# Kernel optimization log

Measured on AMD Instinct MI355X. Metric: run time of the kernel, lower is better.

Reference implementation:

```python
import jax, jax.numpy as jnp
import numpy as np
import math

E, H, FFN, NQ = 1024, 16, 4096, 8
B, T = 2, 2048
EPS = 1e-5

def layernorm(x, g, b):
    mu = jnp.mean(x, axis=-1, keepdims=True)
    var = jnp.mean(jnp.square(x - mu), axis=-1, keepdims=True)
    return (x - mu) * jax.lax.rsqrt(var + EPS) * g + b

def setup_inputs() -> dict:
    key = jax.random.key(0)
    ks = jax.random.split(key, 8)
    x = jax.random.normal(ks[0], (B, T, E), dtype=jnp.float32)
    mask = jnp.ones((B, T, T), dtype=bool)
    # constant quantum measurement output: PauliZ expectations of a fixed
    # RandomLayer circuit applied to |0..0> (independent of the input tokens)
    q_out = jax.random.uniform(ks[1], (NQ,), minval=-1.0, maxval=1.0, dtype=jnp.float32)
    s1 = 1.0 / math.sqrt(NQ)
    w1 = jax.random.uniform(ks[2], (NQ, FFN), minval=-s1, maxval=s1, dtype=jnp.float32)
    b1 = jnp.zeros((FFN,), dtype=jnp.float32)
    s2 = 1.0 / math.sqrt(FFN)
    w2 = jax.random.uniform(ks[3], (FFN, E), minval=-s2, maxval=s2, dtype=jnp.float32)
    b2 = jnp.zeros((E,), dtype=jnp.float32)
    g1 = jnp.ones((E,), dtype=jnp.float32); be1 = jnp.zeros((E,), dtype=jnp.float32)
    g2 = jnp.ones((E,), dtype=jnp.float32); be2 = jnp.zeros((E,), dtype=jnp.float32)
    return dict(x=x, mask=mask, q_out=q_out, w1=w1, b1=b1, w2=w2, b2=b2,
                g1=g1, be1=be1, g2=g2, be2=be2)

def reference(x, mask, q_out, w1, b1, w2, b2, g1, be1, g2, be2):
    b, t, e = x.shape
    d_k = e // H
    # q = k = v = head-split x (module has no QKV projections)
    q = x.reshape(b, t, H, d_k).transpose(0, 2, 1, 3)  # [B,H,T,d_k]
    scores = jnp.einsum('bhqd,bhkd->bhqk', q, q) / math.sqrt(d_k)
    scores = jnp.where(mask[:, None, :, :], scores, -1e9)
    attn = jax.nn.softmax(scores, axis=-1)
    out = jnp.einsum('bhqk,bhkd->bhqd', attn, q)
    attn_out = out.transpose(0, 2, 1, 3).reshape(b, t, e)
    x1 = layernorm(x + attn_out, g1, be1)
    # quantum FFN: constant measurement vector broadcast over all tokens
    h = jnp.broadcast_to(q_out, (b, t, NQ))
    h = jnp.dot(h, w1) + b1
    ffn_out = jnp.dot(jax.nn.relu(h), w2) + b2
    return layernorm(x1 + ffn_out, g2, be2)
```

## Files before the change

### kernel.cpp

```cpp
#include <hip/hip_runtime.h>

#define E_   1024
#define H_   16
#define DK_  64
#define FFN_ 4096
#define NQ_  8
#define B_   2
#define T_   2048
#define QBLK 64
#define KVBLK 64
#define NT_  (T_ / KVBLK)

#define NPART 256
#define ROWS_PER_PART (FFN_ / NPART)

typedef __attribute__((ext_vector_type(8))) __bf16 bf16x8;
typedef __attribute__((ext_vector_type(4))) float f32x4;

__device__ __forceinline__ __bf16 tobf(float f) { return (__bf16)f; }

__device__ __forceinline__ unsigned pk2(float a, float b) {
  union { __bf16 h; unsigned short u; } ua, ub;
  ua.h = (__bf16)a; ub.h = (__bf16)b;
  return (unsigned)ua.u | ((unsigned)ub.u << 16);
}

__global__ __launch_bounds__(256)
void cvt_kernel(const float* __restrict__ x, __bf16* __restrict__ xbf) {
  const size_t base = ((size_t)blockIdx.x * 256 + threadIdx.x) * 8;
  float4 a = *reinterpret_cast<const float4*>(x + base);
  float4 b = *reinterpret_cast<const float4*>(x + base + 4);
  bf16x8 v;
  v[0] = tobf(a.x); v[1] = tobf(a.y); v[2] = tobf(a.z); v[3] = tobf(a.w);
  v[4] = tobf(b.x); v[5] = tobf(b.y); v[6] = tobf(b.z); v[7] = tobf(b.w);
  *reinterpret_cast<bf16x8*>(xbf + base) = v;
}

__global__ __launch_bounds__(256)
void ffn_part_kernel(const float* __restrict__ q_out, const float* __restrict__ w1,
                     const float* __restrict__ b1, const float* __restrict__ w2,
                     float* __restrict__ part) {
  __shared__ float h[ROWS_PER_PART];
  const int tid = threadIdx.x;
  const int p = blockIdx.x;
  const int f0 = p * ROWS_PER_PART;
  if (tid < ROWS_PER_PART) {
    const int f = f0 + tid;
    float a = b1[f];
#pragma unroll
    for (int n = 0; n < NQ_; ++n) a += q_out[n] * w1[n * FFN_ + f];
    h[tid] = fmaxf(a, 0.f);
  }
  __syncthreads();
  float4 acc = {0.f, 0.f, 0.f, 0.f};
#pragma unroll
  for (int j = 0; j < ROWS_PER_PART; ++j) {
    const float hf = h[j];
    float4 w = reinterpret_cast<const float4*>(w2 + (size_t)(f0 + j) * E_)[tid];
    acc.x += hf * w.x; acc.y += hf * w.y; acc.z += hf * w.z; acc.w += hf * w.w;
  }
  reinterpret_cast<float4*>(part + (size_t)p * E_)[tid] = acc;
}

__global__ __launch_bounds__(256)
void ffn_reduce_kernel(const float* __restrict__ part, const float* __restrict__ b2,
                       float* __restrict__ ffn_c) {
  const int e = blockIdx.x * 256 + threadIdx.x;
  float a = b2[e];
  for (int r = 0; r < NPART; ++r) a += part[(size_t)r * E_ + e];
  ffn_c[e] = a;
}

__global__ __launch_bounds__(128)
void attn_kernel(const __bf16* __restrict__ xbf, float* __restrict__ out) {
  __shared__ __bf16 Kt[KVBLK][DK_ + 8];
  __shared__ __bf16 VtF[DK_ * KVBLK];
  __shared__ __bf16 Pl[2][32][DK_ + 8];

  const int tid  = threadIdx.x;
  const int wave = tid >> 6;
  const int lane = tid & 63;
  const int l16  = lane & 15;
  const int lhi  = lane >> 4;

  const int bh = blockIdx.y;
  const int b  = bh >> 4;
  const int h  = bh & 15;
  const int qbase = blockIdx.x * QBLK;
  const __bf16* xb = xbf + (size_t)b * T_ * E_ + h * DK_;

  bf16x8 qa[2][2];
  {
    const __bf16 sc = (__bf16)0.125f;
#pragma unroll
    for (int g = 0; g < 2; ++g) {
      const __bf16* qrow = xb + (size_t)(qbase + wave * 32 + g * 16 + l16) * E_;
      bf16x8 v0 = *reinterpret_cast<const bf16x8*>(qrow + lhi * 8);
      bf16x8 v1 = *reinterpret_cast<const bf16x8*>(qrow + 32 + lhi * 8);
#pragma unroll
      for (int j = 0; j < 8; ++j) { v0[j] *= sc; v1[j] *= sc; }
      qa[g][0] = v0; qa[g][1] = v1;
    }
  }

  f32x4 acc[2][4];
#pragma unroll
  for (int g = 0; g < 2; ++g)
#pragma unroll
    for (int td = 0; td < 4; ++td) acc[g][td] = (f32x4){0.f, 0.f, 0.f, 0.f};
  float lg0 = 0.f, lg1 = 0.f;

  const int kp = tid >> 3;
  const int d0 = (tid & 7) * 8;
  const __bf16* kvbase = xb + (size_t)(4 * kp) * E_ + d0;

  uint4 pr[4];
#pragma unroll
  for (int r = 0; r < 4; ++r)
    pr[r] = *reinterpret_cast<const uint4*>(kvbase + (size_t)r * E_);

  for (int t = 0; t < NT_; ++t) {
    __syncthreads();
    {
#pragma unroll
      for (int r = 0; r < 4; ++r)
        *reinterpret_cast<uint4*>(&Kt[4 * kp + r][d0]) = pr[r];
      union U4 { uint4 v; unsigned short s[8]; } u0, u1, u2, u3;
      u0.v = pr[0]; u1.v = pr[1]; u2.v = pr[2]; u3.v = pr[3];
#pragma unroll
      for (int j = 0; j < 8; ++j) {
        const int d = d0 + j;
        uint2 w;
        w.x = (unsigned)u0.s[j] | ((unsigned)u1.s[j] << 16);
        w.y = (unsigned)u2.s[j] | ((unsigned)u3.s[j] << 16);
        const int byte = d * 128 + ((8 * kp) ^ ((((d & 7) ^ ((d >> 3) & 7))) << 4));
        *reinterpret_cast<uint2*>(reinterpret_cast<char*>(VtF) + byte) = w;
      }
    }
    if (t + 1 < NT_) {
      const __bf16* nb = kvbase + (size_t)(t + 1) * KVBLK * E_;
#pragma unroll
      for (int r = 0; r < 4; ++r)
        pr[r] = *reinterpret_cast<const uint4*>(nb + (size_t)r * E_);
    }
    __syncthreads();

    f32x4 s0[4], s1[4];
#pragma unroll
    for (int tn = 0; tn < 4; ++tn) {
      bf16x8 ka0 = *reinterpret_cast<const bf16x8*>(&Kt[tn * 16 + l16][lhi * 8]);
      bf16x8 ka1 = *reinterpret_cast<const bf16x8*>(&Kt[tn * 16 + l16][32 + lhi * 8]);
      f32x4 c0 = (f32x4){0.f, 0.f, 0.f, 0.f};
      c0 = __builtin_amdgcn_mfma_f32_16x16x32_bf16(ka0, qa[0][0], c0, 0, 0, 0);
      c0 = __builtin_amdgcn_mfma_f32_16x16x32_bf16(ka1, qa[0][1], c0, 0, 0, 0);
      s0[tn] = c0;
      f32x4 c1 = (f32x4){0.f, 0.f, 0.f, 0.f};
      c1 = __builtin_amdgcn_mfma_f32_16x16x32_bf16(ka0, qa[1][0], c1, 0, 0, 0);
      c1 = __builtin_amdgcn_mfma_f32_16x16x32_bf16(ka1, qa[1][1], c1, 0, 0, 0);
      s1[tn] = c1;
    }

#pragma unroll
    for (int tn = 0; tn < 4; ++tn) {
      float p0 = __expf(s0[tn][0]), p1 = __expf(s0[tn][1]);
      float p2 = __expf(s0[tn][2]), p3 = __expf(s0[tn][3]);
      lg0 += (p0 + p1) + (p2 + p3);
      uint2 w; w.x = pk2(p0, p1); w.y = pk2(p2, p3);
      *reinterpret_cast<uint2*>(&Pl[wave][l16][tn * 16 + lhi * 4]) = w;
    }
#pragma unroll
    for (int tn = 0; tn < 4; ++tn) {
      float p0 = __expf(s1[tn][0]), p1 = __expf(s1[tn][1]);
      float p2 = __expf(s1[tn][2]), p3 = __expf(s1[tn][3]);
      lg1 += (p0 + p1) + (p2 + p3);
      uint2 w; w.x = pk2(p0, p1); w.y = pk2(p2, p3);
      *reinterpret_cast<uint2*>(&Pl[wave][16 + l16][tn * 16 + lhi * 4]) = w;
    }
    asm volatile("s_waitcnt lgkmcnt(0)" ::: "memory");

#pragma unroll
    for (int kb = 0; kb < 2; ++kb) {
      bf16x8 pa0 = *reinterpret_cast<const bf16x8*>(&Pl[wave][l16][kb * 32 + lhi * 8]);
      bf16x8 pa1 = *reinterpret_cast<const bf16x8*>(&Pl[wave][16 + l16][kb * 32 + lhi * 8]);
#pragma unroll
      for (int td = 0; td < 4; ++td) {
        const int d = td * 16 + l16;
        const int byte = d * 128 +
                         ((kb * 64 + lhi * 16) ^ (((d & 7) ^ ((d >> 3) & 7)) << 4));
        bf16x8 vb = *reinterpret_cast<const bf16x8*>(
            reinterpret_cast<const char*>(VtF) + byte);
        acc[0][td] = __builtin_amdgcn_mfma_f32_16x16x32_bf16(pa0, vb, acc[0][td], 0, 0, 0);
        acc[1][td] = __builtin_amdgcn_mfma_f32_16x16x32_bf16(pa1, vb, acc[1][td], 0, 0, 0);
      }
    }
  }

  lg0 += __shfl_xor(lg0, 16); lg0 += __shfl_xor(lg0, 32);
  lg1 += __shfl_xor(lg1, 16); lg1 += __shfl_xor(lg1, 32);
  float inv0[4], inv1[4];
#pragma unroll
  for (int i = 0; i < 4; ++i) {
    inv0[i] = 1.f / __shfl(lg0, lhi * 4 + i);
    inv1[i] = 1.f / __shfl(lg1, lhi * 4 + i);
  }
#pragma unroll
  for (int td = 0; td < 4; ++td)
#pragma unroll
    for (int i = 0; i < 4; ++i) {
      const int col = h * DK_ + td * 16 + l16;
      const size_t r0 = (size_t)b * T_ + qbase + wave * 32 + lhi * 4 + i;
      out[r0 * E_ + col]             = acc[0][td][i] * inv0[i];
      out[(r0 + 16) * E_ + col]      = acc[1][td][i] * inv1[i];
    }
}

__device__ __forceinline__ float block_sum(float v, float* redrow, int lane, int wave) {
#pragma unroll
  for (int off = 1; off < 64; off <<= 1) v += __shfl_xor(v, off);
  if (lane == 0) redrow[wave] = v;
  __syncthreads();
  return redrow[0] + redrow[1] + redrow[2] + redrow[3];
}

__global__ __launch_bounds__(256)
void ln_kernel(const float* __restrict__ x, const float* __restrict__ ffn_c,
               const float* __restrict__ g1, const float* __restrict__ be1,
               const float* __restrict__ g2, const float* __restrict__ be2,
               float* io) {
  __shared__ float red[4][4];
  const int row = blockIdx.x;
  const int tid = threadIdx.x;
  const int lane = tid & 63, wave = tid >> 6;
  const float* xr = x + (size_t)row * E_;
  float* ior = io + (size_t)row * E_;

  float4 xv = reinterpret_cast<const float4*>(xr)[tid];
  float4 av = reinterpret_cast<const float4*>(ior)[tid];
  float v[4] = {xv.x + av.x, xv.y + av.y, xv.z + av.z, xv.w + av.w};

  float mu1 = block_sum(v[0] + v[1] + v[2] + v[3], red[0], lane, wave) * (1.f / E_);
  float q1 = 0.f;
#pragma unroll
  for (int j = 0; j < 4; ++j) { float d = v[j] - mu1; q1 += d * d; }
  float var1 = block_sum(q1, red[1], lane, wave) * (1.f / E_);
  float rs1 = rsqrtf(var1 + 1e-5f);

  const int e0 = tid * 4;
  float y[4];
#pragma unroll
  for (int j = 0; j < 4; ++j)
    y[j] = (v[j] - mu1) * rs1 * g1[e0 + j] + be1[e0 + j] + ffn_c[e0 + j];

  float mu2 = block_sum(y[0] + y[1] + y[2] + y[3], red[2], lane, wave) * (1.f / E_);
  float q2 = 0.f;
#pragma unroll
  for (int j = 0; j < 4; ++j) { float d = y[j] - mu2; q2 += d * d; }
  float var2 = block_sum(q2, red[3], lane, wave) * (1.f / E_);
  float rs2 = rsqrtf(var2 + 1e-5f);

  float4 o;
  o.x = (y[0] - mu2) * rs2 * g2[e0 + 0] + be2[e0 + 0];
  o.y = (y[1] - mu2) * rs2 * g2[e0 + 1] + be2[e0 + 1];
  o.z = (y[2] - mu2) * rs2 * g2[e0 + 2] + be2[e0 + 2];
  o.w = (y[3] - mu2) * rs2 * g2[e0 + 3] + be2[e0 + 3];
  reinterpret_cast<float4*>(ior)[tid] = o;
}

extern "C" void kernel_launch(void* const* d_in, const int* in_sizes, int n_in,
                              void* d_out, int out_size, void* d_ws, size_t ws_size,
                              hipStream_t stream) {
  (void)in_sizes; (void)n_in; (void)out_size; (void)ws_size;
  const float* x     = (const float*)d_in[0];
  const float* q_out = (const float*)d_in[2];
  const float* w1    = (const float*)d_in[3];
  const float* b1    = (const float*)d_in[4];
  const float* w2    = (const float*)d_in[5];
  const float* b2    = (const float*)d_in[6];
  const float* g1    = (const float*)d_in[7];
  const float* be1   = (const float*)d_in[8];
  const float* g2    = (const float*)d_in[9];
  const float* be2   = (const float*)d_in[10];
  float* out   = (float*)d_out;
  float* ffn_c = (float*)d_ws;
  float* part  = (float*)d_ws + E_;
  __bf16* xbf  = (__bf16*)((float*)d_ws + E_ + NPART * E_);

  cvt_kernel<<<(B_ * T_ * E_) / (256 * 8), 256, 0, stream>>>(x, xbf);
  ffn_part_kernel<<<NPART, 256, 0, stream>>>(q_out, w1, b1, w2, part);
  ffn_reduce_kernel<<<E_ / 256, 256, 0, stream>>>(part, b2, ffn_c);
  dim3 ag(T_ / QBLK, B_ * H_);
  attn_kernel<<<ag, 128, 0, stream>>>(xbf, out);
  ln_kernel<<<B_ * T_, 256, 0, stream>>>(x, ffn_c, g1, be1, g2, be2, out);
}
```

Baseline: 97.97 us.

## Double-buffer K/V tiles in LDS and widen attention block to four waves

The attention kernel now runs 256 threads over 128 query rows per block, so each K/V tile loaded into LDS is shared by four waves instead of two. K and transposed V are double-buffered, which leaves one barrier per iteration: the next tile's global loads are issued before compute and written to the spare buffer afterwards. s_setprio is raised around the MFMA sections. The cost is twice the LDS per block and half as many blocks in the grid, which may reduce occupancy and CU coverage.

```diff
diff --git a/kernel.cpp b/kernel.cpp
--- a/kernel.cpp
+++ b/kernel.cpp
@@ -7,7 +7,7 @@
 #define NQ_  8
 #define B_   2
 #define T_   2048
-#define QBLK 64
+#define QBLK 128
 #define KVBLK 64
 #define NT_  (T_ / KVBLK)
 
@@ -71,11 +71,11 @@
   ffn_c[e] = a;
 }
 
-__global__ __launch_bounds__(128)
+__global__ __launch_bounds__(256)
 void attn_kernel(const __bf16* __restrict__ xbf, float* __restrict__ out) {
-  __shared__ __bf16 Kt[KVBLK][DK_ + 8];
-  __shared__ __bf16 VtF[DK_ * KVBLK];
-  __shared__ __bf16 Pl[2][32][DK_ + 8];
+  __shared__ __bf16 Kt[2][KVBLK][DK_ + 8];
+  __shared__ __bf16 VtF[2][DK_ * KVBLK];
+  __shared__ __bf16 Pl[4][32][DK_ + 8];
 
   const int tid  = threadIdx.x;
   const int wave = tid >> 6;
@@ -112,44 +112,45 @@
 
   const int kp = tid >> 3;
   const int d0 = (tid & 7) * 8;
-  const __bf16* kvbase = xb + (size_t)(4 * kp) * E_ + d0;
-
-  uint4 pr[4];
-#pragma unroll
-  for (int r = 0; r < 4; ++r)
-    pr[r] = *reinterpret_cast<const uint4*>(kvbase + (size_t)r * E_);
+  const __bf16* kvbase = xb + (size_t)(2 * kp) * E_ + d0;
+
+  {
+    uint4 p0 = *reinterpret_cast<const uint4*>(kvbase);
+    uint4 p1 = *reinterpret_cast<const uint4*>(kvbase + E_);
+    *reinterpret_cast<uint4*>(&Kt[0][2 * kp][d0])     = p0;
+    *reinterpret_cast<uint4*>(&Kt[0][2 * kp + 1][d0]) = p1;
+    union U4 { uint4 v; unsigned short s[8]; } u0, u1;
+    u0.v = p0; u1.v = p1;
+#pragma unroll
+    for (int j = 0; j < 8; ++j) {
+      const int d = d0 + j;
+      const unsigned w = (unsigned)u0.s[j] | ((unsigned)u1.s[j] << 16);
+      const int byte = d * 128 + ((4 * kp) ^ ((((d & 7) ^ ((d >> 3) & 7))) << 4));
+      *reinterpret_cast<unsigned*>(reinterpret_cast<char*>(&VtF[0][0]) + byte) = w;
+    }
+  }
+  __syncthreads();
 
   for (int t = 0; t < NT_; ++t) {
-    __syncthreads();
-    {
-#pragma unroll
-      for (int r = 0; r < 4; ++r)
-        *reinterpret_cast<uint4*>(&Kt[4 * kp + r][d0]) = pr[r];
-      union U4 { uint4 v; unsigned short s[8]; } u0, u1, u2, u3;
-      u0.v = pr[0]; u1.v = pr[1]; u2.v = pr[2]; u3.v = pr[3];
-#pragma unroll
-      for (int j = 0; j < 8; ++j) {
-        const int d = d0 + j;
-        uint2 w;
-        w.x = (unsigned)u0.s[j] | ((unsigned)u1.s[j] << 16);
-        w.y = (unsigned)u2.s[j] | ((unsigned)u3.s[j] << 16);
-        const int byte = d * 128 + ((8 * kp) ^ ((((d & 7) ^ ((d >> 3) & 7))) << 4));
-        *reinterpret_cast<uint2*>(reinterpret_cast<char*>(VtF) + byte) = w;
-      }
-    }
-    if (t + 1 < NT_) {
+    const int cur = t & 1;
+    const __bf16* Ktc = &Kt[cur][0][0];
+    const char*   Vtc = reinterpret_cast<const char*>(&VtF[cur][0]);
+
+    uint4 nr0, nr1;
+    const bool have_next = (t + 1 < NT_);
+    if (have_next) {
       const __bf16* nb = kvbase + (size_t)(t + 1) * KVBLK * E_;
-#pragma unroll
-      for (int r = 0; r < 4; ++r)
-        pr[r] = *reinterpret_cast<const uint4*>(nb + (size_t)r * E_);
-    }
-    __syncthreads();
+      nr0 = *reinterpret_cast<const uint4*>(nb);
+      nr1 = *reinterpret_cast<const uint4*>(nb + E_);
+    }
 
     f32x4 s0[4], s1[4];
+    __builtin_amdgcn_s_setprio(1);
 #pragma unroll
     for (int tn = 0; tn < 4; ++tn) {
-      bf16x8 ka0 = *reinterpret_cast<const bf16x8*>(&Kt[tn * 16 + l16][lhi * 8]);
-      bf16x8 ka1 = *reinterpret_cast<const bf16x8*>(&Kt[tn * 16 + l16][32 + lhi * 8]);
+      const __bf16* kr = Ktc + (tn * 16 + l16) * (DK_ + 8);
+      bf16x8 ka0 = *reinterpret_cast<const bf16x8*>(kr + lhi * 8);
+      bf16x8 ka1 = *reinterpret_cast<const bf16x8*>(kr + 32 + lhi * 8);
       f32x4 c0 = (f32x4){0.f, 0.f, 0.f, 0.f};
       c0 = __builtin_amdgcn_mfma_f32_16x16x32_bf16(ka0, qa[0][0], c0, 0, 0, 0);
       c0 = __builtin_amdgcn_mfma_f32_16x16x32_bf16(ka1, qa[0][1], c0, 0, 0, 0);
@@ -159,6 +160,7 @@
       c1 = __builtin_amdgcn_mfma_f32_16x16x32_bf16(ka1, qa[1][1], c1, 0, 0, 0);
       s1[tn] = c1;
     }
+    __builtin_amdgcn_s_setprio(0);
 
 #pragma unroll
     for (int tn = 0; tn < 4; ++tn) {
@@ -167,17 +169,15 @@
       lg0 += (p0 + p1) + (p2 + p3);
       uint2 w; w.x = pk2(p0, p1); w.y = pk2(p2, p3);
       *reinterpret_cast<uint2*>(&Pl[wave][l16][tn * 16 + lhi * 4]) = w;
-    }
-#pragma unroll
-    for (int tn = 0; tn < 4; ++tn) {
-      float p0 = __expf(s1[tn][0]), p1 = __expf(s1[tn][1]);
-      float p2 = __expf(s1[tn][2]), p3 = __expf(s1[tn][3]);
-      lg1 += (p0 + p1) + (p2 + p3);
-      uint2 w; w.x = pk2(p0, p1); w.y = pk2(p2, p3);
-      *reinterpret_cast<uint2*>(&Pl[wave][16 + l16][tn * 16 + lhi * 4]) = w;
+      float q0 = __expf(s1[tn][0]), q1 = __expf(s1[tn][1]);
+      float q2 = __expf(s1[tn][2]), q3 = __expf(s1[tn][3]);
+      lg1 += (q0 + q1) + (q2 + q3);
+      uint2 u; u.x = pk2(q0, q1); u.y = pk2(q2, q3);
+      *reinterpret_cast<uint2*>(&Pl[wave][16 + l16][tn * 16 + lhi * 4]) = u;
     }
     asm volatile("s_waitcnt lgkmcnt(0)" ::: "memory");
 
+    __builtin_amdgcn_s_setprio(1);
 #pragma unroll
     for (int kb = 0; kb < 2; ++kb) {
       bf16x8 pa0 = *reinterpret_cast<const bf16x8*>(&Pl[wave][l16][kb * 32 + lhi * 8]);
@@ -187,12 +187,29 @@
         const int d = td * 16 + l16;
         const int byte = d * 128 +
                          ((kb * 64 + lhi * 16) ^ (((d & 7) ^ ((d >> 3) & 7)) << 4));
-        bf16x8 vb = *reinterpret_cast<const bf16x8*>(
-            reinterpret_cast<const char*>(VtF) + byte);
-        acc[0][td] = __builtin_amdgcn_mfma_f32_16x16x32_bf16(pa0, vb, acc[0][td], 0, 0, 0);
-        acc[1][td] = __builtin_amdgcn_mfma_f32_16x16x32_bf16(pa1, vb, acc[1][td], 0, 0, 0);
+        bf16x8 vv = *reinterpret_cast<const bf16x8*>(Vtc + byte);
+        acc[0][td] = __builtin_amdgcn_mfma_f32_16x16x32_bf16(pa0, vv, acc[0][td], 0, 0, 0);
+        acc[1][td] = __builtin_amdgcn_mfma_f32_16x16x32_bf16(pa1, vv, acc[1][td], 0, 0, 0);
       }
     }
+    __builtin_amdgcn_s_setprio(0);
+
+    if (have_next) {
+      const int nxt = cur ^ 1;
+      *reinterpret_cast<uint4*>(&Kt[nxt][2 * kp][d0])     = nr0;
+      *reinterpret_cast<uint4*>(&Kt[nxt][2 * kp + 1][d0]) = nr1;
+      union U4 { uint4 v; unsigned short s[8]; } u0, u1;
+      u0.v = nr0; u1.v = nr1;
+      char* vb = reinterpret_cast<char*>(&VtF[nxt][0]);
+#pragma unroll
+      for (int j = 0; j < 8; ++j) {
+        const int d = d0 + j;
+        const unsigned w = (unsigned)u0.s[j] | ((unsigned)u1.s[j] << 16);
+        const int byte = d * 128 + ((4 * kp) ^ ((((d & 7) ^ ((d >> 3) & 7))) << 4));
+        *reinterpret_cast<unsigned*>(vb + byte) = w;
+      }
+    }
+    __syncthreads();
   }
 
   lg0 += __shfl_xor(lg0, 16); lg0 += __shfl_xor(lg0, 32);
@@ -209,8 +226,8 @@
     for (int i = 0; i < 4; ++i) {
       const int col = h * DK_ + td * 16 + l16;
       const size_t r0 = (size_t)b * T_ + qbase + wave * 32 + lhi * 4 + i;
-      out[r0 * E_ + col]             = acc[0][td][i] * inv0[i];
-      out[(r0 + 16) * E_ + col]      = acc[1][td][i] * inv1[i];
+      out[r0 * E_ + col]        = acc[0][td][i] * inv0[i];
+      out[(r0 + 16) * E_ + col] = acc[1][td][i] * inv1[i];
     }
 }
 
@@ -289,6 +306,6 @@
   ffn_part_kernel<<<NPART, 256, 0, stream>>>(q_out, w1, b1, w2, part);
   ffn_reduce_kernel<<<E_ / 256, 256, 0, stream>>>(part, b2, ffn_c);
   dim3 ag(T_ / QBLK, B_ * H_);
-  attn_kernel<<<ag, 128, 0, stream>>>(xbf, out);
+  attn_kernel<<<ag, 256, 0, stream>>>(xbf, out);
   ln_kernel<<<B_ * T_, 256, 0, stream>>>(x, ffn_c, g1, be1, g2, be2, out);
 }
```

Result: faster. 94.56 us (-3.5%).
